# Optimization experiments

Measured on AMD Instinct MI355X. Metric: run time of the kernel, lower is better.

The kernel has to match this reference:

```python
import jax, jax.numpy as jnp
import numpy as np

N = 4096      # batch_size
D = 256       # projection dim
TEMP = 0.5    # temperature


def setup_inputs() -> dict:
    key = jax.random.key(0)
    k1, k2 = jax.random.split(key)
    return {
        "emb_i": jax.random.normal(k1, (N, D), dtype=jnp.float32),
        "emb_j": jax.random.normal(k2, (N, D), dtype=jnp.float32),
    }


def reference(emb_i, emb_j):
    # L2-normalize rows (F.normalize, dim=1)
    z_i = emb_i / jnp.maximum(jnp.linalg.norm(emb_i, axis=1, keepdims=True), 1e-12)
    z_j = emb_j / jnp.maximum(jnp.linalg.norm(emb_j, axis=1, keepdims=True), 1e-12)
    rep = jnp.concatenate([z_i, z_j], axis=0)            # [2N, D]

    # cosine similarity of unit vectors == dot product -> GEMM instead of O(N^2 D) broadcast
    sim = rep @ rep.T                                    # [2N, 2N]

    # positives: diag(sim, +N) and diag(sim, -N) are both sum(z_i*z_j, axis=1)
    pos_ij = jnp.sum(z_i * z_j, axis=1)                  # [N]
    positives = jnp.concatenate([pos_ij, pos_ij], axis=0)  # [2N]

    # mask keeps exactly the two cross-view blocks (main diagonal lies in same-view blocks)
    idx = jnp.arange(2 * N)
    mask = (idx[:, None] < N) != (idx[None, :] < N)      # [2N, 2N] bool

    nominator = jnp.exp(positives / TEMP)                # [2N]
    denominator = jnp.sum(jnp.where(mask, jnp.exp(sim / TEMP), 0.0), axis=1)  # [2N]

    loss_partial = -jnp.log(nominator / (0.5 * denominator))
    return jnp.sum(loss_partial) / (2 * N)
```

## Files before the change

kernel.cpp:

```cpp
#include <hip/hip_runtime.h>
#include <math.h>

#define NROWS 4096
#define DDIM  256
#define BM 128
#define BN 128
#define BK 64
#define LOG2E2 2.8853900817779268f

typedef __attribute__((ext_vector_type(8))) short short8;
typedef __attribute__((ext_vector_type(4))) float f32x4;

__device__ __forceinline__ unsigned short f2bf(float f) {
    unsigned int u = __float_as_uint(f);
    u += 0x7fffu + ((u >> 16) & 1u);
    return (unsigned short)(u >> 16);
}

__device__ __forceinline__ float exp2_fast(float x) {
#if __has_builtin(__builtin_amdgcn_exp2f)
    return __builtin_amdgcn_exp2f(x);
#else
    return exp2f(x);
#endif
}

#define GLOAD_LDS16(gsrc, ldst)                                          \
    __builtin_amdgcn_global_load_lds(                                    \
        (__attribute__((address_space(1))) void*)(gsrc),                 \
        (__attribute__((address_space(3))) void*)(ldst), 16, 0, 0)

__global__ __launch_bounds__(256) void normalize_kernel(
    const float* __restrict__ emb_i, const float* __restrict__ emb_j,
    unsigned short* __restrict__ zi, unsigned short* __restrict__ zj,
    float* __restrict__ pos)
{
    const int wave = threadIdx.x >> 6;
    const int lane = threadIdx.x & 63;
    const int row  = blockIdx.x * 4 + wave;

    const float4 vi = *((const float4*)(emb_i + (size_t)row * DDIM) + lane);
    const float4 vj = *((const float4*)(emb_j + (size_t)row * DDIM) + lane);

    float ssi = vi.x*vi.x + vi.y*vi.y + vi.z*vi.z + vi.w*vi.w;
    float ssj = vj.x*vj.x + vj.y*vj.y + vj.z*vj.z + vj.w*vj.w;
    #pragma unroll
    for (int m = 1; m < 64; m <<= 1) {
        ssi += __shfl_xor(ssi, m);
        ssj += __shfl_xor(ssj, m);
    }
    const float ri = 1.0f / fmaxf(sqrtf(ssi), 1e-12f);
    const float rj = 1.0f / fmaxf(sqrtf(ssj), 1e-12f);

    const float zix = vi.x*ri, ziy = vi.y*ri, ziz = vi.z*ri, ziw = vi.w*ri;
    const float zjx = vj.x*rj, zjy = vj.y*rj, zjz = vj.z*rj, zjw = vj.w*rj;

    float p = zix*zjx + ziy*zjy + ziz*zjz + ziw*zjw;
    #pragma unroll
    for (int m = 1; m < 64; m <<= 1) p += __shfl_xor(p, m);
    if (lane == 0) pos[row] = p;

    ushort4 oi = { f2bf(zix*LOG2E2), f2bf(ziy*LOG2E2), f2bf(ziz*LOG2E2), f2bf(ziw*LOG2E2) };
    ushort4 oj = { f2bf(zjx), f2bf(zjy), f2bf(zjz), f2bf(zjw) };
    *((ushort4*)(zi + (size_t)row * DDIM) + lane) = oi;
    *((ushort4*)(zj + (size_t)row * DDIM) + lane) = oj;
}

__global__ __launch_bounds__(256) void gemm_fused_kernel(
    const unsigned short* __restrict__ zi, const unsigned short* __restrict__ zj,
    float* __restrict__ rowsum, float* __restrict__ colsum)
{
    __shared__ unsigned short As[BM * BK];
    __shared__ unsigned short Bs[BM * BK];

    const int tid  = threadIdx.x;
    const int lane = tid & 63;
    const int wave = tid >> 6;
    const int g    = lane >> 4;
    const int fr   = lane & 15;
    const int wr   = wave >> 1;
    const int wc   = wave & 1;
    const int bm   = blockIdx.x * BM;
    const int bn   = blockIdx.y * BN;

    f32x4 acc[4][4] = {};

    for (int k0 = 0; k0 < DDIM; k0 += BK) {
        #pragma unroll
        for (int it = 0; it < 4; ++it) {
            const int idx  = it * 256 + tid;
            const int row  = idx >> 3;
            const int slot = idx & 7;
            const int soff = ((slot ^ (row & 7)) << 3);
            const int loff = (it * 256 + wave * 64) << 3;
            GLOAD_LDS16(zi + (size_t)(bm + row) * DDIM + k0 + soff, As + loff);
            GLOAD_LDS16(zj + (size_t)(bn + row) * DDIM + k0 + soff, Bs + loff);
        }
        __syncthreads();

        #pragma unroll
        for (int kk = 0; kk < 2; ++kk) {
            short8 a[4], b[4];
            #pragma unroll
            for (int mi = 0; mi < 4; ++mi) {
                const int row  = wr * 64 + mi * 16 + fr;
                const int slot = kk * 4 + g;
                a[mi] = *(const short8*)&As[row * 64 + ((slot ^ (row & 7)) << 3)];
            }
            #pragma unroll
            for (int ni = 0; ni < 4; ++ni) {
                const int row  = wc * 64 + ni * 16 + fr;
                const int slot = kk * 4 + g;
                b[ni] = *(const short8*)&Bs[row * 64 + ((slot ^ (row & 7)) << 3)];
            }
            #pragma unroll
            for (int mi = 0; mi < 4; ++mi)
                #pragma unroll
                for (int ni = 0; ni < 4; ++ni)
                    acc[mi][ni] = __builtin_amdgcn_mfma_f32_16x16x32_bf16(
                        a[mi], b[ni], acc[mi][ni], 0, 0, 0);
        }
        __syncthreads();
    }

    float rp[4][4];
    float cp[4] = {0.f, 0.f, 0.f, 0.f};
    #pragma unroll
    for (int mi = 0; mi < 4; ++mi)
        #pragma unroll
        for (int j = 0; j < 4; ++j) rp[mi][j] = 0.f;

    #pragma unroll
    for (int mi = 0; mi < 4; ++mi)
        #pragma unroll
        for (int ni = 0; ni < 4; ++ni)
            #pragma unroll
            for (int j = 0; j < 4; ++j) {
                const float e = exp2_fast(acc[mi][ni][j]);
                rp[mi][j] += e;
                cp[ni]    += e;
            }

    #pragma unroll
    for (int mi = 0; mi < 4; ++mi)
        #pragma unroll
        for (int j = 0; j < 4; ++j) {
            float v = rp[mi][j];
            v += __shfl_xor(v, 1); v += __shfl_xor(v, 2);
            v += __shfl_xor(v, 4); v += __shfl_xor(v, 8);
            if (fr == 0)
                atomicAdd(&rowsum[bm + wr * 64 + mi * 16 + g * 4 + j], v);
        }

    #pragma unroll
    for (int ni = 0; ni < 4; ++ni) {
        float v = cp[ni];
        v += __shfl_xor(v, 16); v += __shfl_xor(v, 32);
        if (g == 0)
            atomicAdd(&colsum[bn + wc * 64 + ni * 16 + fr], v);
    }
}

__global__ __launch_bounds__(256) void finalize_kernel(
    const float* __restrict__ pos, const float* __restrict__ rowsum,
    const float* __restrict__ colsum, float* __restrict__ out)
{
    float s = 0.0f;
    for (int r = threadIdx.x; r < NROWS; r += 256) {
        s += -4.0f * pos[r] + logf(0.5f * rowsum[r]) + logf(0.5f * colsum[r]);
    }
    __shared__ float part[4];
    #pragma unroll
    for (int m = 1; m < 64; m <<= 1) s += __shfl_xor(s, m);
    if ((threadIdx.x & 63) == 0) part[threadIdx.x >> 6] = s;
    __syncthreads();
    if (threadIdx.x == 0)
        out[0] = (part[0] + part[1] + part[2] + part[3]) / (2.0f * NROWS);
}

extern "C" void kernel_launch(void* const* d_in, const int* in_sizes, int n_in,
                              void* d_out, int out_size, void* d_ws, size_t ws_size,
                              hipStream_t stream)
{
    const float* emb_i = (const float*)d_in[0];
    const float* emb_j = (const float*)d_in[1];

    unsigned short* zi = (unsigned short*)d_ws;
    unsigned short* zj = zi + (size_t)NROWS * DDIM;
    float* pos    = (float*)(zj + (size_t)NROWS * DDIM);
    float* rowsum = pos + NROWS;
    float* colsum = rowsum + NROWS;

    hipMemsetAsync(rowsum, 0, 2 * NROWS * sizeof(float), stream);

    normalize_kernel<<<NROWS / 4, 256, 0, stream>>>(emb_i, emb_j, zi, zj, pos);

    dim3 grid(NROWS / BM, NROWS / BN);
    gemm_fused_kernel<<<grid, 256, 0, stream>>>(zi, zj, rowsum, colsum);

    finalize_kernel<<<1, 256, 0, stream>>>(pos, rowsum, colsum, (float*)d_out);
}
```

Before: 87.41 us.

## Use 256x256 tiles with 512 threads and double-buffered LDS staging

Doubles the GEMM block tile to 256x256, runs eight waves per block, and double-buffers the A and B LDS tiles so that global-to-LDS loads for the next K-slice overlap MFMA work on the current one. The aim is more operand reuse per staged byte and fewer row and column-sum atomics per output element. The trade-off is a grid of only 256 blocks at one block per CU, plus heavier LDS use of 128 KB per block. It also merges the two logs in the finalize kernel into one.

```diff
diff --git a/kernel.cpp b/kernel.cpp
--- a/kernel.cpp
+++ b/kernel.cpp
@@ -3,8 +3,8 @@
 
 #define NROWS 4096
 #define DDIM  256
-#define BM 128
-#define BN 128
+#define BM 256
+#define BN 256
 #define BK 64
 #define LOG2E2 2.8853900817779268f
 
@@ -66,92 +66,92 @@
     *((ushort4*)(zj + (size_t)row * DDIM) + lane) = oj;
 }
 
-__global__ __launch_bounds__(256) void gemm_fused_kernel(
+__global__ __launch_bounds__(512) void gemm_fused_kernel(
     const unsigned short* __restrict__ zi, const unsigned short* __restrict__ zj,
     float* __restrict__ rowsum, float* __restrict__ colsum)
 {
-    __shared__ unsigned short As[BM * BK];
-    __shared__ unsigned short Bs[BM * BK];
+    __shared__ unsigned short As[2][BM * BK];
+    __shared__ unsigned short Bs[2][BM * BK];
 
     const int tid  = threadIdx.x;
     const int lane = tid & 63;
     const int wave = tid >> 6;
     const int g    = lane >> 4;
     const int fr   = lane & 15;
-    const int wr   = wave >> 1;
-    const int wc   = wave & 1;
+    const int wr   = wave >> 2;
+    const int wc   = wave & 3;
     const int bm   = blockIdx.x * BM;
     const int bn   = blockIdx.y * BN;
 
-    f32x4 acc[4][4] = {};
-
-    for (int k0 = 0; k0 < DDIM; k0 += BK) {
+    f32x4 acc[8][4] = {};
+
+    const int srow0 = tid >> 3;
+    const int soff  = (((tid & 7) ^ (srow0 & 7)) << 3);
+
+    auto stage = [&](int buf, int k0) {
         #pragma unroll
         for (int it = 0; it < 4; ++it) {
-            const int idx  = it * 256 + tid;
-            const int row  = idx >> 3;
-            const int slot = idx & 7;
-            const int soff = ((slot ^ (row & 7)) << 3);
-            const int loff = (it * 256 + wave * 64) << 3;
-            GLOAD_LDS16(zi + (size_t)(bm + row) * DDIM + k0 + soff, As + loff);
-            GLOAD_LDS16(zj + (size_t)(bn + row) * DDIM + k0 + soff, Bs + loff);
+            const int row = it * 64 + srow0;
+            const int lb  = (it * 512 + wave * 64) << 3;
+            GLOAD_LDS16(zi + (size_t)(bm + row) * DDIM + k0 + soff, &As[buf][lb]);
+            GLOAD_LDS16(zj + (size_t)(bn + row) * DDIM + k0 + soff, &Bs[buf][lb]);
         }
-        __syncthreads();
-
+    };
+
+    auto compute = [&](int buf) {
         #pragma unroll
         for (int kk = 0; kk < 2; ++kk) {
-            short8 a[4], b[4];
-            #pragma unroll
-            for (int mi = 0; mi < 4; ++mi) {
-                const int row  = wr * 64 + mi * 16 + fr;
-                const int slot = kk * 4 + g;
-                a[mi] = *(const short8*)&As[row * 64 + ((slot ^ (row & 7)) << 3)];
-            }
-            #pragma unroll
-            for (int ni = 0; ni < 4; ++ni) {
-                const int row  = wc * 64 + ni * 16 + fr;
-                const int slot = kk * 4 + g;
-                b[ni] = *(const short8*)&Bs[row * 64 + ((slot ^ (row & 7)) << 3)];
-            }
-            #pragma unroll
-            for (int mi = 0; mi < 4; ++mi)
+            const int coff = (((kk * 4 + g) ^ (fr & 7)) << 3);
+            short8 a[8], b[4];
+            #pragma unroll
+            for (int mi = 0; mi < 8; ++mi)
+                a[mi] = *(const short8*)&As[buf][(wr * 128 + mi * 16 + fr) * BK + coff];
+            #pragma unroll
+            for (int ni = 0; ni < 4; ++ni)
+                b[ni] = *(const short8*)&Bs[buf][(wc * 64 + ni * 16 + fr) * BK + coff];
+            #pragma unroll
+            for (int mi = 0; mi < 8; ++mi)
                 #pragma unroll
                 for (int ni = 0; ni < 4; ++ni)
                     acc[mi][ni] = __builtin_amdgcn_mfma_f32_16x16x32_bf16(
                         a[mi], b[ni], acc[mi][ni], 0, 0, 0);
         }
-        __syncthreads();
-    }
-
-    float rp[4][4];
+    };
+
+    stage(0, 0);
+    __syncthreads();
+    stage(1, BK);
+    compute(0);
+    __syncthreads();
+    stage(0, 2 * BK);
+    compute(1);
+    __syncthreads();
+    stage(1, 3 * BK);
+    compute(0);
+    __syncthreads();
+    compute(1);
+
     float cp[4] = {0.f, 0.f, 0.f, 0.f};
     #pragma unroll
-    for (int mi = 0; mi < 4; ++mi)
-        #pragma unroll
-        for (int j = 0; j < 4; ++j) rp[mi][j] = 0.f;
-
-    #pragma unroll
-    for (int mi = 0; mi < 4; ++mi)
+    for (int mi = 0; mi < 8; ++mi) {
+        float rpj[4] = {0.f, 0.f, 0.f, 0.f};
         #pragma unroll
         for (int ni = 0; ni < 4; ++ni)
             #pragma unroll
             for (int j = 0; j < 4; ++j) {
                 const float e = exp2_fast(acc[mi][ni][j]);
-                rp[mi][j] += e;
-                cp[ni]    += e;
+                rpj[j]  += e;
+                cp[ni]  += e;
             }
-
-    #pragma unroll
-    for (int mi = 0; mi < 4; ++mi)
         #pragma unroll
         for (int j = 0; j < 4; ++j) {
-            float v = rp[mi][j];
+            float v = rpj[j];
             v += __shfl_xor(v, 1); v += __shfl_xor(v, 2);
             v += __shfl_xor(v, 4); v += __shfl_xor(v, 8);
             if (fr == 0)
-                atomicAdd(&rowsum[bm + wr * 64 + mi * 16 + g * 4 + j], v);
+                atomicAdd(&rowsum[bm + wr * 128 + mi * 16 + g * 4 + j], v);
         }
-
+    }
     #pragma unroll
     for (int ni = 0; ni < 4; ++ni) {
         float v = cp[ni];
@@ -167,7 +167,7 @@
 {
     float s = 0.0f;
     for (int r = threadIdx.x; r < NROWS; r += 256) {
-        s += -4.0f * pos[r] + logf(0.5f * rowsum[r]) + logf(0.5f * colsum[r]);
+        s += -4.0f * pos[r] + logf(0.25f * rowsum[r] * colsum[r]);
     }
     __shared__ float part[4];
     #pragma unroll
@@ -196,7 +196,7 @@
     normalize_kernel<<<NROWS / 4, 256, 0, stream>>>(emb_i, emb_j, zi, zj, pos);
 
     dim3 grid(NROWS / BM, NROWS / BN);
-    gemm_fused_kernel<<<grid, 256, 0, stream>>>(zi, zj, rowsum, colsum);
+    gemm_fused_kernel<<<grid, 512, 0, stream>>>(zi, zj, rowsum, colsum);
 
     finalize_kernel<<<1, 256, 0, stream>>>(pos, rowsum, colsum, (float*)d_out);
 }
```

After: 93.12 us. 6.5% more time.

## Load full K into LDS, fold memset into normalize, merge finalize logs

Applied to the files above, without the earlier changes.

The GEMM kernel now stages the whole 256-wide K dimension of both tiles into LDS in one pass, keeping the same XOR swizzle, so the per-K-step barriers and loop disappear. The separate hipMemsetAsync is removed; the normalize kernel zeroes the rowsum/colsum buffers instead, saving a launch. The finalize kernel uses 512 threads and computes one log of the product instead of two logs. The exchange is 128KB of LDS per block, which limits each CU to a single resident block and removes any overlap between loads and MFMA work across blocks.

```diff
diff --git a/kernel.cpp b/kernel.cpp
--- a/kernel.cpp
+++ b/kernel.cpp
@@ -5,7 +5,6 @@
 #define DDIM  256
 #define BM 128
 #define BN 128
-#define BK 64
 #define LOG2E2 2.8853900817779268f
 
 typedef __attribute__((ext_vector_type(8))) short short8;
@@ -33,8 +32,10 @@
 __global__ __launch_bounds__(256) void normalize_kernel(
     const float* __restrict__ emb_i, const float* __restrict__ emb_j,
     unsigned short* __restrict__ zi, unsigned short* __restrict__ zj,
-    float* __restrict__ pos)
-{
+    float* __restrict__ pos, float* __restrict__ sums )
+{
+    if (threadIdx.x < 8) sums[blockIdx.x * 8 + threadIdx.x] = 0.0f;
+
     const int wave = threadIdx.x >> 6;
     const int lane = threadIdx.x & 63;
     const int row  = blockIdx.x * 4 + wave;
@@ -70,8 +71,8 @@
     const unsigned short* __restrict__ zi, const unsigned short* __restrict__ zj,
     float* __restrict__ rowsum, float* __restrict__ colsum)
 {
-    __shared__ unsigned short As[BM * BK];
-    __shared__ unsigned short Bs[BM * BK];
+    __shared__ unsigned short As[BM * DDIM];
+    __shared__ unsigned short Bs[BN * DDIM];
 
     const int tid  = threadIdx.x;
     const int lane = tid & 63;
@@ -85,42 +86,38 @@
 
     f32x4 acc[4][4] = {};
 
-    for (int k0 = 0; k0 < DDIM; k0 += BK) {
-        #pragma unroll
-        for (int it = 0; it < 4; ++it) {
-            const int idx  = it * 256 + tid;
-            const int row  = idx >> 3;
-            const int slot = idx & 7;
-            const int soff = ((slot ^ (row & 7)) << 3);
-            const int loff = (it * 256 + wave * 64) << 3;
-            GLOAD_LDS16(zi + (size_t)(bm + row) * DDIM + k0 + soff, As + loff);
-            GLOAD_LDS16(zj + (size_t)(bn + row) * DDIM + k0 + soff, Bs + loff);
+    #pragma unroll
+    for (int it = 0; it < 16; ++it) {
+        const int L    = it * 256 + tid;
+        const int row  = L >> 5;
+        const int sl   = L & 31;
+        const int soff = ((sl ^ (row & 7)) << 3);
+        const int lb   = (it * 256 + wave * 64) << 3;
+        GLOAD_LDS16(zi + (size_t)(bm + row) * DDIM + soff, As + lb);
+        GLOAD_LDS16(zj + (size_t)(bn + row) * DDIM + soff, Bs + lb);
+    }
+    __syncthreads();
+
+    #pragma unroll
+    for (int kk = 0; kk < 8; ++kk) {
+        const int cs = kk * 4 + g;
+        short8 a[4], b[4];
+        #pragma unroll
+        for (int mi = 0; mi < 4; ++mi) {
+            const int row = wr * 64 + mi * 16 + fr;
+            a[mi] = *(const short8*)&As[row * DDIM + ((cs ^ (fr & 7)) << 3)];
         }
-        __syncthreads();
-
-        #pragma unroll
-        for (int kk = 0; kk < 2; ++kk) {
-            short8 a[4], b[4];
+        #pragma unroll
+        for (int ni = 0; ni < 4; ++ni) {
+            const int row = wc * 64 + ni * 16 + fr;
+            b[ni] = *(const short8*)&Bs[row * DDIM + ((cs ^ (fr & 7)) << 3)];
+        }
+        #pragma unroll
+        for (int mi = 0; mi < 4; ++mi)
             #pragma unroll
-            for (int mi = 0; mi < 4; ++mi) {
-                const int row  = wr * 64 + mi * 16 + fr;
-                const int slot = kk * 4 + g;
-                a[mi] = *(const short8*)&As[row * 64 + ((slot ^ (row & 7)) << 3)];
-            }
-            #pragma unroll
-            for (int ni = 0; ni < 4; ++ni) {
-                const int row  = wc * 64 + ni * 16 + fr;
-                const int slot = kk * 4 + g;
-                b[ni] = *(const short8*)&Bs[row * 64 + ((slot ^ (row & 7)) << 3)];
-            }
-            #pragma unroll
-            for (int mi = 0; mi < 4; ++mi)
-                #pragma unroll
-                for (int ni = 0; ni < 4; ++ni)
-                    acc[mi][ni] = __builtin_amdgcn_mfma_f32_16x16x32_bf16(
-                        a[mi], b[ni], acc[mi][ni], 0, 0, 0);
-        }
-        __syncthreads();
+            for (int ni = 0; ni < 4; ++ni)
+                acc[mi][ni] = __builtin_amdgcn_mfma_f32_16x16x32_bf16(
+                    a[mi], b[ni], acc[mi][ni], 0, 0, 0);
     }
 
     float rp[4][4];
@@ -161,21 +158,25 @@
     }
 }
 
-__global__ __launch_bounds__(256) void finalize_kernel(
+__global__ __launch_bounds__(512) void finalize_kernel(
     const float* __restrict__ pos, const float* __restrict__ rowsum,
     const float* __restrict__ colsum, float* __restrict__ out)
 {
     float s = 0.0f;
-    for (int r = threadIdx.x; r < NROWS; r += 256) {
-        s += -4.0f * pos[r] + logf(0.5f * rowsum[r]) + logf(0.5f * colsum[r]);
-    }
-    __shared__ float part[4];
+    for (int r = threadIdx.x; r < NROWS; r += 512) {
+        s += -4.0f * pos[r] + logf(0.25f * rowsum[r] * colsum[r]);
+    }
+    __shared__ float part[8];
     #pragma unroll
     for (int m = 1; m < 64; m <<= 1) s += __shfl_xor(s, m);
     if ((threadIdx.x & 63) == 0) part[threadIdx.x >> 6] = s;
     __syncthreads();
-    if (threadIdx.x == 0)
-        out[0] = (part[0] + part[1] + part[2] + part[3]) / (2.0f * NROWS);
+    if (threadIdx.x == 0) {
+        float t = 0.f;
+        #pragma unroll
+        for (int w = 0; w < 8; ++w) t += part[w];
+        out[0] = t / (2.0f * NROWS);
+    }
 }
 
 extern "C" void kernel_launch(void* const* d_in, const int* in_sizes, int n_in,
@@ -191,12 +192,10 @@
     float* rowsum = pos + NROWS;
     float* colsum = rowsum + NROWS;
 
-    hipMemsetAsync(rowsum, 0, 2 * NROWS * sizeof(float), stream);
-
-    normalize_kernel<<<NROWS / 4, 256, 0, stream>>>(emb_i, emb_j, zi, zj, pos);
+    normalize_kernel<<<NROWS / 4, 256, 0, stream>>>(emb_i, emb_j, zi, zj, pos, rowsum);
 
     dim3 grid(NROWS / BM, NROWS / BN);
     gemm_fused_kernel<<<grid, 256, 0, stream>>>(zi, zj, rowsum, colsum);
 
-    finalize_kernel<<<1, 256, 0, stream>>>(pos, rowsum, colsum, (float*)d_out);
-}
+    finalize_kernel<<<1, 512, 0, stream>>>(pos, rowsum, colsum, (float*)d_out);
+}
```

Result: slower. 93.26 us (+6.7%).
